# Kernel optimization log

Hardware: AMD Instinct MI355X
Metric: run time of the kernel (lower is better)

Reference implementation:

```python
import jax, jax.numpy as jnp
import numpy as np

U_N = 100000
I_N = 50000
EMB_DIM = 64
L_N = 3          # number of propagation layers
NNZ = 4_800_000  # edges in the normalized bipartite graph (avg degree ~32)


def setup_inputs() -> dict:
    key = jax.random.key(0)
    k_u, k_i, k_r, k_c, k_v = jax.random.split(key, 5)
    N = U_N + I_N
    # Xavier-uniform-ish embedding init
    lim = float(np.sqrt(6.0 / (U_N + EMB_DIM)))
    user_emb = jax.random.uniform(k_u, (U_N, EMB_DIM), jnp.float32, -lim, lim)
    lim_i = float(np.sqrt(6.0 / (I_N + EMB_DIM)))
    item_emb = jax.random.uniform(k_i, (I_N, EMB_DIM), jnp.float32, -lim_i, lim_i)
    # COO sparse graph over all N = u_n + i_n nodes
    row = jax.random.randint(k_r, (NNZ,), 0, N, jnp.int32)
    col = jax.random.randint(k_c, (NNZ,), 0, N, jnp.int32)
    # emulate symmetric-normalized adjacency values ~ 1/deg so propagation stays bounded
    vals = jax.random.uniform(k_v, (NNZ,), jnp.float32) * (1.0 / 32.0)
    return {"user_emb": user_emb, "item_emb": item_emb, "row": row, "col": col, "vals": vals}


def reference(user_emb, item_emb, row, col, vals):
    N = user_emb.shape[0] + item_emb.shape[0]
    all_emb = jnp.concatenate([user_emb, item_emb], axis=0)  # [N, D]
    emb0 = all_emb
    acc = all_emb  # running sum over layer embeddings (layer 0 included)
    x = all_emb
    for _ in range(L_N):
        # SpMM: out[r] += vals[e] * x[col[e]] for each edge e with row[e] == r
        x = jax.ops.segment_sum(vals[:, None] * x[col], row, num_segments=N)
        acc = acc + x
    out = acc / (L_N + 1)  # mean over stacked layer embeddings
    return (emb0, out)
```

## Files before the change

kernel.cpp:

```cpp
#include <hip/hip_runtime.h>

#define U_N 100000
#define I_N 50000
#define N_NODES 150000
#define EMB_D 64
#define NNZ 4800000
#define ND (N_NODES * EMB_D)
#define ND4 (ND / 4)
#define UD4 (U_N * EMB_D / 4)

#define RPB 1024
#define NB ((N_NODES + RPB - 1) / RPB)
#define TILE 4096
#define NTILE ((NNZ + TILE - 1) / TILE)

__device__ __forceinline__ unsigned short f2bf(float f) {
    unsigned int u = __float_as_uint(f);
    unsigned int r = (u + 0x7FFFu + ((u >> 16) & 1u)) >> 16;
    return (unsigned short)r;
}
__device__ __forceinline__ float bf2f(unsigned short h) {
    return __uint_as_float((unsigned int)h << 16);
}

__global__ void k_init(const float4* __restrict__ u, const float4* __restrict__ it,
                       float4* __restrict__ emb0, ushort4* __restrict__ hb0) {
    int i = blockIdx.x * blockDim.x + threadIdx.x;
    if (i >= ND4) return;
    float4 v = (i < UD4) ? u[i] : it[i - UD4];
    emb0[i] = v;
    ushort4 h;
    h.x = f2bf(v.x); h.y = f2bf(v.y); h.z = f2bf(v.z); h.w = f2bf(v.w);
    hb0[i] = h;
}

__global__ void k_bucket_hist(const int* __restrict__ row, int* __restrict__ bhist) {
    __shared__ int lh[NB];
    int t = threadIdx.x;
    for (int i = t; i < NB; i += 256) lh[i] = 0;
    __syncthreads();
    int base = blockIdx.x * TILE;
    int cnt = min(TILE, NNZ - base);
    for (int i = t; i < cnt; i += 256)
        atomicAdd(&lh[row[base + i] >> 10], 1);
    __syncthreads();
    for (int i = t; i < NB; i += 256)
        if (lh[i]) atomicAdd(&bhist[i], lh[i]);
}

__global__ void k_bucket_scan(const int* __restrict__ bhist, int* __restrict__ bbase,
                              int* __restrict__ bcur) {
    if (threadIdx.x == 0 && blockIdx.x == 0) {
        int run = 0;
        for (int i = 0; i < NB; ++i) { bbase[i] = run; bcur[i] = run; run += bhist[i]; }
        bbase[NB] = run;
    }
}

__global__ void k_partition(const int* __restrict__ row, const int* __restrict__ col,
                            const float* __restrict__ vals, int* __restrict__ bcur,
                            int2* __restrict__ tmp) {
    __shared__ int2 stage[TILE];
    __shared__ unsigned char stageB[TILE];
    __shared__ int hist[NB];
    __shared__ int scn[NB];
    __shared__ int gbase[NB];
    __shared__ int sums[256];
    int t = threadIdx.x;
    for (int i = t; i < NB; i += 256) hist[i] = 0;
    __syncthreads();
    int base = blockIdx.x * TILE;
    int cnt = min(TILE, NNZ - base);

    int  myb[16];
    int  myslot[16];
    int2 myp[16];
#pragma unroll
    for (int j = 0; j < 16; ++j) {
        int i = t + j * 256;
        myb[j] = -1;
        if (i < cnt) {
            int e = base + i;
            int r = row[e];
            int b = r >> 10;
            myb[j] = b;
            myp[j] = make_int2(((r & (RPB - 1)) << 18) | col[e], __float_as_int(vals[e]));
            myslot[j] = atomicAdd(&hist[b], 1);
        }
    }
    __syncthreads();
    int v = (t < NB) ? hist[t] : 0;
    sums[t] = v;
    __syncthreads();
    for (int off = 1; off < 256; off <<= 1) {
        int add = (t >= off) ? sums[t - off] : 0;
        __syncthreads();
        sums[t] += add;
        __syncthreads();
    }
    if (t < NB) scn[t] = sums[t] - v;
    __syncthreads();
    if (t < NB && v > 0) gbase[t] = atomicAdd(&bcur[t], v);
    __syncthreads();
#pragma unroll
    for (int j = 0; j < 16; ++j) {
        if (myb[j] >= 0) {
            int pos = scn[myb[j]] + myslot[j];
            stage[pos] = myp[j];
            stageB[pos] = (unsigned char)myb[j];
        }
    }
    __syncthreads();
    for (int i = t; i < cnt; i += 256) {
        int b = stageB[i];
        tmp[gbase[b] + (i - scn[b])] = stage[i];
    }
}

__global__ void k_bucket_csr(const int* __restrict__ bbase, const int2* __restrict__ tmp,
                             int2* __restrict__ edges, int* __restrict__ rp) {
    __shared__ int lh[RPB];
    __shared__ int lsc[RPB];
    int b = blockIdx.x, t = threadIdx.x;
    int s0 = bbase[b], s1 = bbase[b + 1];
    int n = s1 - s0;
    lh[t] = 0;
    __syncthreads();
    for (int i = t; i < n; i += 1024)
        atomicAdd(&lh[(unsigned)tmp[s0 + i].x >> 18], 1);
    __syncthreads();
    int v = lh[t];
    lsc[t] = v;
    __syncthreads();
    for (int off = 1; off < 1024; off <<= 1) {
        int add = (t >= off) ? lsc[t - off] : 0;
        __syncthreads();
        lsc[t] += add;
        __syncthreads();
    }
    int excl = lsc[t] - v;
    int r = b * RPB + t;
    if (r < N_NODES) rp[r] = s0 + excl;
    if (b == NB - 1 && t == 0) rp[N_NODES] = NNZ;
    __syncthreads();
    lh[t] = excl;
    __syncthreads();
    for (int i = t; i < n; i += 1024) {
        int2 p = tmp[s0 + i];
        int rl = (unsigned)p.x >> 18;
        int pos = s0 + atomicAdd(&lh[rl], 1);
        edges[pos] = make_int2(p.x & 0x3FFFF, p.y);
    }
}

__device__ __forceinline__ float row_dot(const int* __restrict__ rp,
                                         const int2* __restrict__ edges,
                                         const unsigned short* __restrict__ x,
                                         int wid, int lane) {
    int start = __builtin_amdgcn_readfirstlane(rp[wid]);
    int end   = __builtin_amdgcn_readfirstlane(rp[wid + 1]);
    float s0 = 0.f, s1 = 0.f, s2 = 0.f, s3 = 0.f;
    int e = start;
    for (; e + 8 <= end; e += 8) {
        int2 E[8];
#pragma unroll
        for (int j = 0; j < 8; ++j) E[j] = edges[e + j];
        float g[8];
#pragma unroll
        for (int j = 0; j < 8; ++j) g[j] = bf2f(x[(size_t)E[j].x * EMB_D + lane]);
        s0 += __int_as_float(E[0].y) * g[0];
        s1 += __int_as_float(E[1].y) * g[1];
        s2 += __int_as_float(E[2].y) * g[2];
        s3 += __int_as_float(E[3].y) * g[3];
        s0 += __int_as_float(E[4].y) * g[4];
        s1 += __int_as_float(E[5].y) * g[5];
        s2 += __int_as_float(E[6].y) * g[6];
        s3 += __int_as_float(E[7].y) * g[7];
    }
    for (; e < end; ++e) {
        int2 ev = edges[e];
        s0 += __int_as_float(ev.y) * bf2f(x[(size_t)ev.x * EMB_D + lane]);
    }
    return (s0 + s1) + (s2 + s3);
}

__global__ void k_spmm_mid(const int* __restrict__ rp, const int2* __restrict__ edges,
                           const unsigned short* __restrict__ x,
                           unsigned short* __restrict__ y) {
    int wid = blockIdx.x * (blockDim.x >> 6) + (threadIdx.x >> 6);
    if (wid >= N_NODES) return;
    int lane = threadIdx.x & 63;
    float s = row_dot(rp, edges, x, wid, lane);
    y[(size_t)wid * EMB_D + lane] = f2bf(s);
}

__global__ void k_spmm_fin(const int* __restrict__ rp, const int2* __restrict__ edges,
                           const unsigned short* __restrict__ x,
                           const float* __restrict__ emb0,
                           const unsigned short* __restrict__ y1,
                           const unsigned short* __restrict__ y2,
                           float* __restrict__ acc) {
    int wid = blockIdx.x * (blockDim.x >> 6) + (threadIdx.x >> 6);
    if (wid >= N_NODES) return;
    int lane = threadIdx.x & 63;
    float s = row_dot(rp, edges, x, wid, lane);
    size_t o = (size_t)wid * EMB_D + lane;
    acc[o] = (emb0[o] + bf2f(y1[o]) + bf2f(y2[o]) + s) * 0.25f;
}

extern "C" void kernel_launch(void* const* d_in, const int* in_sizes, int n_in,
                              void* d_out, int out_size, void* d_ws, size_t ws_size,
                              hipStream_t stream) {
    const float* user_emb = (const float*)d_in[0];
    const float* item_emb = (const float*)d_in[1];
    const int*   row      = (const int*)d_in[2];
    const int*   col      = (const int*)d_in[3];
    const float* vals     = (const float*)d_in[4];

    float* emb0 = (float*)d_out;
    float* acc  = (float*)d_out + ND;

    int2* tmp   = (int2*)d_ws;
    int2* edges = tmp + NNZ;
    unsigned short* hb2 = (unsigned short*)(edges + NNZ);
    int*  ibase = (int*)(hb2 + ND);
    int*  rp    = ibase;
    int*  bhist = ibase + N_NODES + 1;
    int*  bbase = bhist + NB;
    int*  bcur  = bbase + NB + 1;
    unsigned short* hb0 = (unsigned short*)d_ws;
    unsigned short* hb1 = hb0 + ND;

    const int BLK = 256;
    const int grid_nd = (ND4 + BLK - 1) / BLK;
    const int grid_spmm = (N_NODES * 64 + BLK - 1) / BLK;

    hipMemsetAsync(bhist, 0, NB * sizeof(int), stream);
    k_bucket_hist<<<NTILE, BLK, 0, stream>>>(row, bhist);
    k_bucket_scan<<<1, 64, 0, stream>>>(bhist, bbase, bcur);
    k_partition<<<NTILE, BLK, 0, stream>>>(row, col, vals, bcur, tmp);
    k_bucket_csr<<<NB, 1024, 0, stream>>>(bbase, tmp, edges, rp);

    k_init<<<grid_nd, BLK, 0, stream>>>((const float4*)user_emb,
                                        (const float4*)item_emb,
                                        (float4*)emb0, (ushort4*)hb0);

    k_spmm_mid<<<grid_spmm, BLK, 0, stream>>>(rp, edges, hb0, hb1);
    k_spmm_mid<<<grid_spmm, BLK, 0, stream>>>(rp, edges, hb1, hb2);
    k_spmm_fin<<<grid_spmm, BLK, 0, stream>>>(rp, edges, hb2, emb0, hb1, hb2, acc);
}
```

Before: 625.7 us.

## Presort edges by column bin within row buckets and read bf16 layer-0 in final pass

```diff
diff --git a/kernel.cpp b/kernel.cpp
--- a/kernel.cpp
+++ b/kernel.cpp
@@ -117,7 +117,37 @@
     }
 }
 
-__global__ void k_bucket_csr(const int* __restrict__ bbase, const int2* __restrict__ tmp,
+__global__ void k_colbin(const int* __restrict__ bbase, const int2* __restrict__ tmp,
+                         int2* __restrict__ tmp2) {
+    __shared__ int lh[1024];
+    __shared__ int lsc[1024];
+    int b = blockIdx.x, t = threadIdx.x;
+    int s0 = bbase[b], n = bbase[b + 1] - s0;
+    lh[t] = 0;
+    __syncthreads();
+    for (int i = t; i < n; i += 1024)
+        atomicAdd(&lh[((unsigned)(tmp[s0 + i].x & 0x3FFFF)) >> 10], 1);
+    __syncthreads();
+    int v = lh[t];
+    lsc[t] = v;
+    __syncthreads();
+    for (int off = 1; off < 1024; off <<= 1) {
+        int add = (t >= off) ? lsc[t - off] : 0;
+        __syncthreads();
+        lsc[t] += add;
+        __syncthreads();
+    }
+    lh[t] = lsc[t] - v;
+    __syncthreads();
+    for (int i = t; i < n; i += 1024) {
+        int2 p = tmp[s0 + i];
+        int bin = ((unsigned)(p.x & 0x3FFFF)) >> 10;
+        int pos = s0 + atomicAdd(&lh[bin], 1);
+        tmp2[pos] = p;
+    }
+}
+
+__global__ void k_bucket_csr(const int* __restrict__ bbase, const int2* __restrict__ tmp2,
                              int2* __restrict__ edges, int* __restrict__ rp) {
     __shared__ int lh[RPB];
     __shared__ int lsc[RPB];
@@ -127,7 +157,7 @@
     lh[t] = 0;
     __syncthreads();
     for (int i = t; i < n; i += 1024)
-        atomicAdd(&lh[(unsigned)tmp[s0 + i].x >> 18], 1);
+        atomicAdd(&lh[(unsigned)tmp2[s0 + i].x >> 18], 1);
     __syncthreads();
     int v = lh[t];
     lsc[t] = v;
@@ -146,7 +176,7 @@
     lh[t] = excl;
     __syncthreads();
     for (int i = t; i < n; i += 1024) {
-        int2 p = tmp[s0 + i];
+        int2 p = tmp2[s0 + i];
         int rl = (unsigned)p.x >> 18;
         int pos = s0 + atomicAdd(&lh[rl], 1);
         edges[pos] = make_int2(p.x & 0x3FFFF, p.y);
@@ -196,16 +226,15 @@
 
 __global__ void k_spmm_fin(const int* __restrict__ rp, const int2* __restrict__ edges,
                            const unsigned short* __restrict__ x,
-                           const float* __restrict__ emb0,
+                           const unsigned short* __restrict__ e0,
                            const unsigned short* __restrict__ y1,
-                           const unsigned short* __restrict__ y2,
                            float* __restrict__ acc) {
     int wid = blockIdx.x * (blockDim.x >> 6) + (threadIdx.x >> 6);
     if (wid >= N_NODES) return;
     int lane = threadIdx.x & 63;
     float s = row_dot(rp, edges, x, wid, lane);
     size_t o = (size_t)wid * EMB_D + lane;
-    acc[o] = (emb0[o] + bf2f(y1[o]) + bf2f(y2[o]) + s) * 0.25f;
+    acc[o] = (bf2f(e0[o]) + bf2f(y1[o]) + bf2f(x[o]) + s) * 0.25f;
 }
 
 extern "C" void kernel_launch(void* const* d_in, const int* in_sizes, int n_in,
@@ -221,15 +250,16 @@
     float* acc  = (float*)d_out + ND;
 
     int2* tmp   = (int2*)d_ws;
-    int2* edges = tmp + NNZ;
-    unsigned short* hb2 = (unsigned short*)(edges + NNZ);
-    int*  ibase = (int*)(hb2 + ND);
+    int2* tmp2  = tmp + NNZ;
+    int2* edges = tmp2 + NNZ;
+    int*  ibase = (int*)(edges + NNZ);
     int*  rp    = ibase;
     int*  bhist = ibase + N_NODES + 1;
     int*  bbase = bhist + NB;
     int*  bcur  = bbase + NB + 1;
-    unsigned short* hb0 = (unsigned short*)d_ws;
+    unsigned short* hb0 = (unsigned short*)tmp;
     unsigned short* hb1 = hb0 + ND;
+    unsigned short* hb2 = (unsigned short*)tmp2;
 
     const int BLK = 256;
     const int grid_nd = (ND4 + BLK - 1) / BLK;
@@ -239,13 +269,13 @@
     k_bucket_hist<<<NTILE, BLK, 0, stream>>>(row, bhist);
     k_bucket_scan<<<1, 64, 0, stream>>>(bhist, bbase, bcur);
     k_partition<<<NTILE, BLK, 0, stream>>>(row, col, vals, bcur, tmp);
-    k_bucket_csr<<<NB, 1024, 0, stream>>>(bbase, tmp, edges, rp);
-
+    k_colbin<<<NB, 1024, 0, stream>>>(bbase, tmp, tmp2);
     k_init<<<grid_nd, BLK, 0, stream>>>((const float4*)user_emb,
                                         (const float4*)item_emb,
                                         (float4*)emb0, (ushort4*)hb0);
+    k_bucket_csr<<<NB, 1024, 0, stream>>>(bbase, tmp2, edges, rp);
 
     k_spmm_mid<<<grid_spmm, BLK, 0, stream>>>(rp, edges, hb0, hb1);
     k_spmm_mid<<<grid_spmm, BLK, 0, stream>>>(rp, edges, hb1, hb2);
-    k_spmm_fin<<<grid_spmm, BLK, 0, stream>>>(rp, edges, hb2, emb0, hb1, hb2, acc);
-}
+    k_spmm_fin<<<grid_spmm, BLK, 0, stream>>>(rp, edges, hb2, hb0, hb1, acc);
+}
```

Measured after the change: 675.7 us. +8.0%, slower.
